# Performance work log

Measured on AMD Instinct MI355X. Metric: run time of the kernel, lower is better.

## Reference

```python
import jax, jax.numpy as jnp
import numpy as np

N, C, H, NG = 200000, 256, 4, 512
D = C // H  # head_dim = 64


def setup_inputs() -> dict:
    key = jax.random.key(0)
    ks = jax.random.split(key, 10)
    s = 1.0 / np.sqrt(C)
    inp = {
        "x": jax.random.normal(ks[0], (N, C), dtype=jnp.float32),
        "batch": jnp.sort(jax.random.randint(ks[1], (N,), 0, NG)),
        "Wq": jax.random.uniform(ks[2], (C, C), jnp.float32, -s, s),
        "bq": jnp.zeros((C,), jnp.float32),
        "Wk": jax.random.uniform(ks[3], (C, C), jnp.float32, -s, s),
        "bk": jnp.zeros((C,), jnp.float32),
        "Wv": jax.random.uniform(ks[4], (C, C), jnp.float32, -s, s),
        "bv": jnp.zeros((C,), jnp.float32),
        "Wo": jax.random.uniform(ks[5], (C, C), jnp.float32, -s, s),
        "bo": jnp.zeros((C,), jnp.float32),
    }
    return inp


def reference(x, batch, Wq, bq, Wk, bk, Wv, bv, Wo, bo):
    n = x.shape[0]
    q = (x @ Wq + bq).reshape(n, H, D)
    k = (x @ Wk + bk).reshape(n, H, D)
    v = (x @ Wv + bv).reshape(n, H, D)
    # per-node head-vs-head scores: [N, H, H]
    scores = jnp.einsum("nhd,ngd->nhg", q, k) / jnp.sqrt(jnp.float32(D))
    # segment softmax across nodes within each graph (torch_geometric.utils.softmax)
    seg_max = jax.ops.segment_max(scores, batch, num_segments=NG)
    e = jnp.exp(scores - seg_max[batch])
    seg_sum = jax.ops.segment_sum(e, batch, num_segments=NG)
    att = e / (seg_sum[batch] + 1e-16)
    out = jnp.einsum("nhg,ngd->nhd", att, v).reshape(n, C)
    out = out @ Wo + bo
    return (out, att.mean(axis=1))
```

## Files before the change

kernel.cpp:

```cpp
#include <hip/hip_runtime.h>

#define NN 200000
#define CC 256
#define NG 512

typedef __attribute__((ext_vector_type(8))) __bf16 bf16x8;
typedef __attribute__((ext_vector_type(16))) float f32x16;

typedef unsigned short u16;

#define VWAITN(n) asm volatile("s_waitcnt vmcnt(%0)" :: "i"(n) : "memory")
#define LWAIT0()  asm volatile("s_waitcnt lgkmcnt(0)" ::: "memory")
#define SBAR() __builtin_amdgcn_s_barrier()

__device__ __forceinline__ u16 f2bf(float f) {
  union { float f; unsigned u; } v; v.f = f;
  unsigned u = v.u;
  u += 0x7fffu + ((u >> 16) & 1u);
  return (u16)(u >> 16);
}
__device__ __forceinline__ unsigned pack2(float a, float b) {
  return (unsigned)f2bf(a) | ((unsigned)f2bf(b) << 16);
}
__device__ __forceinline__ float bflo(unsigned u){ union{unsigned u; float f;} x; x.u = u << 16; return x.f; }
__device__ __forceinline__ float bfhi(unsigned u){ union{unsigned u; float f;} x; x.u = u & 0xffff0000u; return x.f; }

__global__ __launch_bounds__(256) void prep_kernel(
    const float* __restrict__ Wq, const float* __restrict__ Wk,
    const float* __restrict__ Wv, const float* __restrict__ Wo,
    u16* __restrict__ Wall) {
  int idx = blockIdx.x * 256 + threadIdx.x;
  int s = idx >> 13;
  int inner = idx & 8191;
  int ks = inner >> 9;
  int l = (inner >> 3) & 63;
  int j = inner & 7;
  int r = l & 31, hi5 = l >> 5;
  int k = ks * 16 + hi5 * 8 + j;
  const float* W; int c0;
  if (s < 16) {
    int p = s >> 3, r4 = s & 7;
    if (r4 < 4) { W = Wk; c0 = r4 * 64 + p * 32; }
    else        { W = Wq; c0 = (r4 - 4) * 64 + p * 32; }
  } else if (s < 24) { W = Wv; c0 = (s - 16) * 32; }
  else               { W = Wo; c0 = (s - 24) * 32; }
  Wall[idx] = f2bf(W[k * 256 + c0 + r]);
}

__global__ __launch_bounds__(256) void seg_bounds_kernel(
    const int* __restrict__ batch, int* __restrict__ seg_start, int n) {
  int i = blockIdx.x * 256 + threadIdx.x;
  if (i >= n) return;
  int a = batch[i];
  int b = (i + 1 < n) ? batch[i + 1] : NG;
  for (int g = a + 1; g <= b; ++g) seg_start[g] = i + 1;
  if (i == 0) for (int g = 0; g <= a; ++g) seg_start[g] = 0;
}

__device__ __forceinline__ void stage_pair(
    const u16* __restrict__ Wall, u16* dst_base, int s0, int w, int lane) {
#pragma unroll
  for (int rep = 0; rep < 8; ++rep) {
    int unit = w * 8 + rep;
    const u16* src = Wall + (size_t)s0 * 8192 + (unit * 64 + lane) * 8;
    u16* dst = dst_base + unit * 512;
    __builtin_amdgcn_global_load_lds(
        (const __attribute__((address_space(1))) void*)src,
        (__attribute__((address_space(3))) void*)dst, 16, 0, 0);
  }
}

__device__ __forceinline__ f32x16 gemm_lds(
    const u16* buf, const bf16x8 xfr[16], int lane) {
  f32x16 a0 = {0.f,0.f,0.f,0.f,0.f,0.f,0.f,0.f,0.f,0.f,0.f,0.f,0.f,0.f,0.f,0.f};
  f32x16 a1 = a0;
#pragma unroll
  for (int ks = 0; ks < 16; ks += 2) {
    bf16x8 f0 = *reinterpret_cast<const bf16x8*>(&buf[(ks * 64 + lane) * 8]);
    bf16x8 f1 = *reinterpret_cast<const bf16x8*>(&buf[((ks + 1) * 64 + lane) * 8]);
    a0 = __builtin_amdgcn_mfma_f32_32x32x16_bf16(f0, xfr[ks], a0, 0, 0, 0);
    a1 = __builtin_amdgcn_mfma_f32_32x32x16_bf16(f1, xfr[ks + 1], a1, 0, 0, 0);
  }
  return a0 + a1;
}

__global__ __launch_bounds__(256, 2) void qkv_scores_kernel(
    const float* __restrict__ x, const u16* __restrict__ Wall,
    const float* __restrict__ bq, const float* __restrict__ bk,
    const float* __restrict__ bv,
    u16* __restrict__ v_out,
    float* __restrict__ scores) {
  __shared__ u16 Wbuf[2][16384];
  __shared__ float biasL[768];

  const int t = threadIdx.x;
  const int w = t >> 6, lane = t & 63;
  const int col = lane & 31, hi5 = lane >> 5;
  int n = blockIdx.x * 128 + w * 32 + col;
  if (n >= NN) n = NN - 1;

  bf16x8 xfr[16];
#pragma unroll
  for (int kb = 0; kb < 16; ++kb) {
    const float* px = x + (size_t)n * CC + kb * 16 + hi5 * 8;
    float4 a0 = *reinterpret_cast<const float4*>(px);
    float4 a1 = *reinterpret_cast<const float4*>(px + 4);
    uint4 u = {pack2(a0.x, a0.y), pack2(a0.z, a0.w),
               pack2(a1.x, a1.y), pack2(a1.z, a1.w)};
    xfr[kb] = *reinterpret_cast<bf16x8*>(&u);
  }
  biasL[t] = bk[t];
  biasL[256 + t] = bq[t];
  biasL[512 + t] = bv[t];

  stage_pair(Wall, Wbuf[0], 0, w, lane);
  LWAIT0();

  float sp[16];
#pragma unroll
  for (int i = 0; i < 16; ++i) sp[i] = 0.f;

  int bi = 0;

#pragma unroll 1
  for (int p = 0; p < 2; ++p) {
    unsigned kph[4][8];
#pragma unroll
    for (int pr = 0; pr < 2; ++pr) {
      VWAITN(0);
      SBAR();
      stage_pair(Wall, Wbuf[bi ^ 1], (p * 4 + pr + 1) * 2, w, lane);
#pragma unroll
      for (int sub = 0; sub < 2; ++sub) {
        const int g = pr * 2 + sub;
        f32x16 acc = gemm_lds(&Wbuf[bi][sub * 8192], xfr, lane);
#pragma unroll
        for (int q = 0; q < 4; ++q) {
          float4 b4 = *reinterpret_cast<const float4*>(
              &biasL[g * 64 + p * 32 + q * 8 + hi5 * 4]);
          kph[g][q * 2]     = pack2(acc[4 * q] + b4.x, acc[4 * q + 1] + b4.y);
          kph[g][q * 2 + 1] = pack2(acc[4 * q + 2] + b4.z, acc[4 * q + 3] + b4.w);
        }
      }
      bi ^= 1;
    }
#pragma unroll
    for (int pr = 0; pr < 2; ++pr) {
      VWAITN(0);
      SBAR();
      stage_pair(Wall, Wbuf[bi ^ 1], (p * 4 + 3 + pr) * 2, w, lane);
#pragma unroll
      for (int sub = 0; sub < 2; ++sub) {
        const int h = pr * 2 + sub;
        f32x16 acc = gemm_lds(&Wbuf[bi][sub * 8192], xfr, lane);
#pragma unroll
        for (int q = 0; q < 4; ++q) {
          float4 b4 = *reinterpret_cast<const float4*>(
              &biasL[256 + h * 64 + p * 32 + q * 8 + hi5 * 4]);
          float q0 = acc[4 * q] + b4.x, q1 = acc[4 * q + 1] + b4.y;
          float q2 = acc[4 * q + 2] + b4.z, q3 = acc[4 * q + 3] + b4.w;
#pragma unroll
          for (int g = 0; g < 4; ++g) {
            unsigned k01 = kph[g][q * 2];
            unsigned k23 = kph[g][q * 2 + 1];
            sp[h * 4 + g] += q0 * bflo(k01) + q1 * bfhi(k01) +
                             q2 * bflo(k23) + q3 * bfhi(k23);
          }
        }
      }
      bi ^= 1;
    }
  }

#pragma unroll
  for (int i = 0; i < 16; ++i) sp[i] += __shfl_xor(sp[i], 32, 64);
  if (hi5 == 0) {
#pragma unroll
    for (int q = 0; q < 4; ++q) {
      float4 o = {sp[q * 4] * 0.125f, sp[q * 4 + 1] * 0.125f,
                  sp[q * 4 + 2] * 0.125f, sp[q * 4 + 3] * 0.125f};
      *reinterpret_cast<float4*>(scores + (size_t)n * 16 + q * 4) = o;
    }
  }

#pragma unroll
  for (int i = 0; i < 4; ++i) {
    if (i == 0) { VWAITN(4); }
    else        { VWAITN(8); }
    SBAR();
    if (i < 3) stage_pair(Wall, Wbuf[bi ^ 1], 18 + 2 * i, w, lane);
#pragma unroll
    for (int sub = 0; sub < 2; ++sub) {
      const int sv = 2 * i + sub;
      f32x16 acc = gemm_lds(&Wbuf[bi][sub * 8192], xfr, lane);
#pragma unroll
      for (int q = 0; q < 4; ++q) {
        int d0 = sv * 32 + q * 8 + hi5 * 4;
        float4 b4 = *reinterpret_cast<const float4*>(&biasL[512 + d0]);
        uint2 pk = {pack2(acc[4 * q] + b4.x, acc[4 * q + 1] + b4.y),
                    pack2(acc[4 * q + 2] + b4.z, acc[4 * q + 3] + b4.w)};
        *reinterpret_cast<uint2*>(v_out + (size_t)n * CC + d0) = pk;
      }
    }
    bi ^= 1;
  }
}

__global__ __launch_bounds__(256) void seg_softmax_kernel(
    const float* __restrict__ scores, const int* __restrict__ seg_start,
    float* __restrict__ seg_max, float* __restrict__ seg_sum) {
  __shared__ float red[256];
  int g = blockIdx.x;
  int s = seg_start[g], e = seg_start[g + 1];
  int t = threadIdx.x;
  int col = t & 15, sub = t >> 4;

  float m = -INFINITY;
  for (int i = s + sub; i < e; i += 16)
    m = fmaxf(m, scores[(size_t)i * 16 + col]);
  red[t] = m;
  __syncthreads();
  for (int step = 8; step >= 1; step >>= 1) {
    if (sub < step) red[t] = fmaxf(red[t], red[t + step * 16]);
    __syncthreads();
  }
  if (t < 16) seg_max[g * 16 + t] = red[t];
  float mcol = red[col];
  __syncthreads();

  float sum = 0.f;
  for (int i = s + sub; i < e; i += 16)
    sum += expf(scores[(size_t)i * 16 + col] - mcol);
  red[t] = sum;
  __syncthreads();
  for (int step = 8; step >= 1; step >>= 1) {
    if (sub < step) red[t] += red[t + step * 16];
    __syncthreads();
  }
  if (t < 16) seg_sum[g * 16 + t] = red[t];
}

__global__ __launch_bounds__(256, 2) void out_kernel(
    const u16* __restrict__ v_bf, const float* __restrict__ scores,
    const int* __restrict__ batch, const float* __restrict__ seg_max,
    const float* __restrict__ seg_sum, const u16* __restrict__ Wall,
    const float* __restrict__ bo, float* __restrict__ out,
    float* __restrict__ att_mean) {
  __shared__ u16 Wbuf[2][16384];
  __shared__ float boL[256];

  const int t = threadIdx.x;
  const int w = t >> 6, lane = t & 63;
  const int col = lane & 31, hi5 = lane >> 5;
  int n = blockIdx.x * 128 + w * 32 + col;
  if (n >= NN) n = NN - 1;

  int b = batch[n];
  float att[16];
#pragma unroll
  for (int q = 0; q < 4; ++q) {
    float4 sc = *reinterpret_cast<const float4*>(scores + (size_t)n * 16 + q * 4);
    float4 mx = *reinterpret_cast<const float4*>(seg_max + b * 16 + q * 4);
    float4 sm = *reinterpret_cast<const float4*>(seg_sum + b * 16 + q * 4);
    att[q * 4 + 0] = expf(sc.x - mx.x) / (sm.x + 1e-16f);
    att[q * 4 + 1] = expf(sc.y - mx.y) / (sm.y + 1e-16f);
    att[q * 4 + 2] = expf(sc.z - mx.z) / (sm.z + 1e-16f);
    att[q * 4 + 3] = expf(sc.w - mx.w) / (sm.w + 1e-16f);
  }

  uint4 vv[4][4];
#pragma unroll
  for (int g = 0; g < 4; ++g)
#pragma unroll
    for (int dw = 0; dw < 4; ++dw)
      vv[g][dw] = *reinterpret_cast<const uint4*>(
          v_bf + (size_t)n * CC + g * 64 + dw * 16 + hi5 * 8);

  boL[t] = bo[t];

  if (hi5 == 0) {
    float4 am;
    am.x = 0.25f * (att[0] + att[4] + att[8] + att[12]);
    am.y = 0.25f * (att[1] + att[5] + att[9] + att[13]);
    am.z = 0.25f * (att[2] + att[6] + att[10] + att[14]);
    am.w = 0.25f * (att[3] + att[7] + att[11] + att[15]);
    *reinterpret_cast<float4*>(att_mean + (size_t)n * 4) = am;
  }

  stage_pair(Wall, Wbuf[0], 24, w, lane);

  bf16x8 oaf[16];
#pragma unroll
  for (int dw = 0; dw < 4; ++dw) {
    float vr[4][8];
#pragma unroll
    for (int g = 0; g < 4; ++g) {
      uint4 u4 = vv[g][dw];
      vr[g][0] = bflo(u4.x); vr[g][1] = bfhi(u4.x);
      vr[g][2] = bflo(u4.y); vr[g][3] = bfhi(u4.y);
      vr[g][4] = bflo(u4.z); vr[g][5] = bfhi(u4.z);
      vr[g][6] = bflo(u4.w); vr[g][7] = bfhi(u4.w);
    }
#pragma unroll
    for (int h = 0; h < 4; ++h) {
      unsigned res[4];
#pragma unroll
      for (int jj = 0; jj < 4; ++jj) {
        float lo = att[h * 4 + 0] * vr[0][2 * jj] + att[h * 4 + 1] * vr[1][2 * jj] +
                   att[h * 4 + 2] * vr[2][2 * jj] + att[h * 4 + 3] * vr[3][2 * jj];
        float hf = att[h * 4 + 0] * vr[0][2 * jj + 1] + att[h * 4 + 1] * vr[1][2 * jj + 1] +
                   att[h * 4 + 2] * vr[2][2 * jj + 1] + att[h * 4 + 3] * vr[3][2 * jj + 1];
        res[jj] = pack2(lo, hf);
      }
      uint4 u = {res[0], res[1], res[2], res[3]};
      oaf[h * 4 + dw] = *reinterpret_cast<bf16x8*>(&u);
    }
  }
  LWAIT0();

  int bi = 0;
#pragma unroll
  for (int i = 0; i < 4; ++i) {
    if (i == 0) { VWAITN(0); }
    else        { VWAITN(8); }
    SBAR();
    if (i < 3) stage_pair(Wall, Wbuf[bi ^ 1], 26 + 2 * i, w, lane);
#pragma unroll
    for (int sub = 0; sub < 2; ++sub) {
      const int so = 2 * i + sub;
      f32x16 acc = gemm_lds(&Wbuf[bi][sub * 8192], oaf, lane);
#pragma unroll
      for (int q = 0; q < 4; ++q) {
        int c0 = so * 32 + q * 8 + hi5 * 4;
        float4 b4 = *reinterpret_cast<const float4*>(&boL[c0]);
        float4 o = {acc[4 * q] + b4.x, acc[4 * q + 1] + b4.y,
                    acc[4 * q + 2] + b4.z, acc[4 * q + 3] + b4.w};
        *reinterpret_cast<float4*>(out + (size_t)n * CC + c0) = o;
      }
    }
    bi ^= 1;
  }
}

extern "C" void kernel_launch(void* const* d_in, const int* in_sizes, int n_in,
                              void* d_out, int out_size, void* d_ws, size_t ws_size,
                              hipStream_t stream) {
  const float* x  = (const float*)d_in[0];
  const int* batch = (const int*)d_in[1];
  const float* Wq = (const float*)d_in[2];
  const float* bq = (const float*)d_in[3];
  const float* Wk = (const float*)d_in[4];
  const float* bk = (const float*)d_in[5];
  const float* Wv = (const float*)d_in[6];
  const float* bv = (const float*)d_in[7];
  const float* Wo = (const float*)d_in[8];
  const float* bo = (const float*)d_in[9];

  char* ws = (char*)d_ws;
  u16*   Wall      = (u16*)ws;
  int*   seg_start = (int*)(ws + 524288);
  float* seg_max   = (float*)(ws + 528384);
  float* seg_sum   = (float*)(ws + 561152);
  float* scores    = (float*)(ws + 593920);
  u16*   v_bf      = (u16*)(ws + 13393920);

  float* out = (float*)d_out;
  float* att_mean = out + (size_t)NN * CC;

  const int NB = (NN + 127) / 128;

  prep_kernel<<<1024, 256, 0, stream>>>(Wq, Wk, Wv, Wo, Wall);
  seg_bounds_kernel<<<(NN + 255) / 256, 256, 0, stream>>>(batch, seg_start, NN);
  qkv_scores_kernel<<<NB, 256, 0, stream>>>(x, Wall, bq, bk, bv, v_bf, scores);
  seg_softmax_kernel<<<NG, 256, 0, stream>>>(scores, seg_start, seg_max, seg_sum);
  out_kernel<<<NB, 256, 0, stream>>>(v_bf, scores, batch, seg_max, seg_sum,
                                     Wall, bo, out, att_mean);
}
```

Measured before the change: 259.1 us.

## Switch QKV and output GEMMs to 16x16x32 MFMA with 512-thread blocks

Both the QKV/score kernel and the output-projection kernel now use 16x16x32 bf16 MFMA tiles instead of 32x32x16, with 8 waves of 16 nodes per 128-node block instead of 4 waves of 32. The weight pre-packing is relaid out to match the new fragment layout, and the LDS staging is spread across all 512 threads. Per-thread register state shrinks, since the x fragment count, the K-partials and the V registers are halved, and a second shuffle step completes the score reduction. The aim is more resident waves and better latency hiding for a bandwidth-heavy kernel. The cost is more MFMA instructions and more LDS fragment reads per output, plus tighter vmcnt bookkeeping.

```diff
diff --git a/kernel.cpp b/kernel.cpp
--- a/kernel.cpp
+++ b/kernel.cpp
@@ -5,7 +5,7 @@
 #define NG 512
 
 typedef __attribute__((ext_vector_type(8))) __bf16 bf16x8;
-typedef __attribute__((ext_vector_type(16))) float f32x16;
+typedef __attribute__((ext_vector_type(4))) float f32x4;
 
 typedef unsigned short u16;
 
@@ -31,12 +31,13 @@
     u16* __restrict__ Wall) {
   int idx = blockIdx.x * 256 + threadIdx.x;
   int s = idx >> 13;
-  int inner = idx & 8191;
-  int ks = inner >> 9;
-  int l = (inner >> 3) & 63;
-  int j = inner & 7;
-  int r = l & 31, hi5 = l >> 5;
-  int k = ks * 16 + hi5 * 8 + j;
+  int r1 = idx & 8191;
+  int sub = r1 >> 12;
+  int r2 = r1 & 4095;
+  int ks = r2 >> 9;
+  int lane = (r2 >> 3) & 63;
+  int j = r2 & 7;
+  int k = ks * 32 + (lane >> 4) * 8 + j;
   const float* W; int c0;
   if (s < 16) {
     int p = s >> 3, r4 = s & 7;
@@ -44,7 +45,7 @@
     else        { W = Wq; c0 = (r4 - 4) * 64 + p * 32; }
   } else if (s < 24) { W = Wv; c0 = (s - 16) * 32; }
   else               { W = Wo; c0 = (s - 24) * 32; }
-  Wall[idx] = f2bf(W[k * 256 + c0 + r]);
+  Wall[idx] = f2bf(W[k * 256 + c0 + sub * 16 + (lane & 15)]);
 }
 
 __global__ __launch_bounds__(256) void seg_bounds_kernel(
@@ -58,33 +59,30 @@
 }
 
 __device__ __forceinline__ void stage_pair(
-    const u16* __restrict__ Wall, u16* dst_base, int s0, int w, int lane) {
-#pragma unroll
-  for (int rep = 0; rep < 8; ++rep) {
-    int unit = w * 8 + rep;
-    const u16* src = Wall + (size_t)s0 * 8192 + (unit * 64 + lane) * 8;
-    u16* dst = dst_base + unit * 512;
+    const u16* __restrict__ Wall, u16* dst_base, int s0, int t) {
+#pragma unroll
+  for (int rep = 0; rep < 4; ++rep) {
+    int unit = rep * 512 + t;
+    const u16* src = Wall + (size_t)s0 * 8192 + unit * 8;
+    u16* dst = dst_base + unit * 8;
     __builtin_amdgcn_global_load_lds(
         (const __attribute__((address_space(1))) void*)src,
         (__attribute__((address_space(3))) void*)dst, 16, 0, 0);
   }
 }
 
-__device__ __forceinline__ f32x16 gemm_lds(
-    const u16* buf, const bf16x8 xfr[16], int lane) {
-  f32x16 a0 = {0.f,0.f,0.f,0.f,0.f,0.f,0.f,0.f,0.f,0.f,0.f,0.f,0.f,0.f,0.f,0.f};
-  f32x16 a1 = a0;
-#pragma unroll
-  for (int ks = 0; ks < 16; ks += 2) {
-    bf16x8 f0 = *reinterpret_cast<const bf16x8*>(&buf[(ks * 64 + lane) * 8]);
-    bf16x8 f1 = *reinterpret_cast<const bf16x8*>(&buf[((ks + 1) * 64 + lane) * 8]);
-    a0 = __builtin_amdgcn_mfma_f32_32x32x16_bf16(f0, xfr[ks], a0, 0, 0, 0);
-    a1 = __builtin_amdgcn_mfma_f32_32x32x16_bf16(f1, xfr[ks + 1], a1, 0, 0, 0);
-  }
-  return a0 + a1;
-}
-
-__global__ __launch_bounds__(256, 2) void qkv_scores_kernel(
+__device__ __forceinline__ f32x4 gemm16(
+    const u16* buf, const bf16x8 xfr[8], int lane) {
+  f32x4 acc = {0.f, 0.f, 0.f, 0.f};
+#pragma unroll
+  for (int ks = 0; ks < 8; ++ks) {
+    bf16x8 af = *reinterpret_cast<const bf16x8*>(&buf[ks * 512 + lane * 8]);
+    acc = __builtin_amdgcn_mfma_f32_16x16x32_bf16(af, xfr[ks], acc, 0, 0, 0);
+  }
+  return acc;
+}
+
+__global__ __launch_bounds__(512, 4) void qkv_scores_kernel(
     const float* __restrict__ x, const u16* __restrict__ Wall,
     const float* __restrict__ bq, const float* __restrict__ bk,
     const float* __restrict__ bv,
@@ -95,25 +93,25 @@
 
   const int t = threadIdx.x;
   const int w = t >> 6, lane = t & 63;
-  const int col = lane & 31, hi5 = lane >> 5;
-  int n = blockIdx.x * 128 + w * 32 + col;
+  const int g4 = lane >> 4;
+  int n = blockIdx.x * 128 + w * 16 + (lane & 15);
   if (n >= NN) n = NN - 1;
 
-  bf16x8 xfr[16];
-#pragma unroll
-  for (int kb = 0; kb < 16; ++kb) {
-    const float* px = x + (size_t)n * CC + kb * 16 + hi5 * 8;
+  bf16x8 xfr[8];
+#pragma unroll
+  for (int ks = 0; ks < 8; ++ks) {
+    const float* px = x + (size_t)n * CC + ks * 32 + g4 * 8;
     float4 a0 = *reinterpret_cast<const float4*>(px);
     float4 a1 = *reinterpret_cast<const float4*>(px + 4);
     uint4 u = {pack2(a0.x, a0.y), pack2(a0.z, a0.w),
                pack2(a1.x, a1.y), pack2(a1.z, a1.w)};
-    xfr[kb] = *reinterpret_cast<bf16x8*>(&u);
-  }
-  biasL[t] = bk[t];
-  biasL[256 + t] = bq[t];
-  biasL[512 + t] = bv[t];
-
-  stage_pair(Wall, Wbuf[0], 0, w, lane);
+    xfr[ks] = *reinterpret_cast<bf16x8*>(&u);
+  }
+  biasL[t < 256 ? t : t] = 0.f;
+  if (t < 256) { biasL[t] = bk[t]; biasL[512 + t] = bv[t]; }
+  else         { biasL[t] = bq[t - 256]; }
+
+  stage_pair(Wall, Wbuf[0], 0, t);
   LWAIT0();
 
   float sp[16];
@@ -124,47 +122,51 @@
 
 #pragma unroll 1
   for (int p = 0; p < 2; ++p) {
-    unsigned kph[4][8];
+    unsigned kph[4][4];
 #pragma unroll
     for (int pr = 0; pr < 2; ++pr) {
+      const int s0 = p * 8 + pr * 2;
       VWAITN(0);
       SBAR();
-      stage_pair(Wall, Wbuf[bi ^ 1], (p * 4 + pr + 1) * 2, w, lane);
-#pragma unroll
-      for (int sub = 0; sub < 2; ++sub) {
-        const int g = pr * 2 + sub;
-        f32x16 acc = gemm_lds(&Wbuf[bi][sub * 8192], xfr, lane);
-#pragma unroll
-        for (int q = 0; q < 4; ++q) {
+      stage_pair(Wall, Wbuf[bi ^ 1], s0 + 2, t);
+#pragma unroll
+      for (int so = 0; so < 2; ++so) {
+        const int g = pr * 2 + so;
+#pragma unroll
+        for (int sub = 0; sub < 2; ++sub) {
+          f32x4 acc = gemm16(&Wbuf[bi][so * 8192 + sub * 4096], xfr, lane);
           float4 b4 = *reinterpret_cast<const float4*>(
-              &biasL[g * 64 + p * 32 + q * 8 + hi5 * 4]);
-          kph[g][q * 2]     = pack2(acc[4 * q] + b4.x, acc[4 * q + 1] + b4.y);
-          kph[g][q * 2 + 1] = pack2(acc[4 * q + 2] + b4.z, acc[4 * q + 3] + b4.w);
+              &biasL[g * 64 + p * 32 + sub * 16 + g4 * 4]);
+          kph[g][sub * 2]     = pack2(acc[0] + b4.x, acc[1] + b4.y);
+          kph[g][sub * 2 + 1] = pack2(acc[2] + b4.z, acc[3] + b4.w);
         }
       }
       bi ^= 1;
     }
 #pragma unroll
     for (int pr = 0; pr < 2; ++pr) {
+      const int s0 = p * 8 + 4 + pr * 2;
       VWAITN(0);
       SBAR();
-      stage_pair(Wall, Wbuf[bi ^ 1], (p * 4 + 3 + pr) * 2, w, lane);
-#pragma unroll
-      for (int sub = 0; sub < 2; ++sub) {
-        const int h = pr * 2 + sub;
-        f32x16 acc = gemm_lds(&Wbuf[bi][sub * 8192], xfr, lane);
-#pragma unroll
-        for (int q = 0; q < 4; ++q) {
+      stage_pair(Wall, Wbuf[bi ^ 1], s0 + 2, t);
+#pragma unroll
+      for (int so = 0; so < 2; ++so) {
+        const int h = pr * 2 + so;
+#pragma unroll
+        for (int sub = 0; sub < 2; ++sub) {
+          f32x4 acc = gemm16(&Wbuf[bi][so * 8192 + sub * 4096], xfr, lane);
           float4 b4 = *reinterpret_cast<const float4*>(
-              &biasL[256 + h * 64 + p * 32 + q * 8 + hi5 * 4]);
-          float q0 = acc[4 * q] + b4.x, q1 = acc[4 * q + 1] + b4.y;
-          float q2 = acc[4 * q + 2] + b4.z, q3 = acc[4 * q + 3] + b4.w;
-#pragma unroll
-          for (int g = 0; g < 4; ++g) {
-            unsigned k01 = kph[g][q * 2];
-            unsigned k23 = kph[g][q * 2 + 1];
-            sp[h * 4 + g] += q0 * bflo(k01) + q1 * bfhi(k01) +
-                             q2 * bflo(k23) + q3 * bfhi(k23);
+              &biasL[256 + h * 64 + p * 32 + sub * 16 + g4 * 4]);
+          float qv[4] = {acc[0] + b4.x, acc[1] + b4.y,
+                         acc[2] + b4.z, acc[3] + b4.w};
+#pragma unroll
+          for (int r = 0; r < 4; ++r) {
+#pragma unroll
+            for (int g = 0; g < 4; ++g) {
+              unsigned kk = kph[g][sub * 2 + (r >> 1)];
+              float kv = (r & 1) ? bfhi(kk) : bflo(kk);
+              sp[h * 4 + g] += qv[r] * kv;
+            }
           }
         }
       }
@@ -173,8 +175,11 @@
   }
 
 #pragma unroll
-  for (int i = 0; i < 16; ++i) sp[i] += __shfl_xor(sp[i], 32, 64);
-  if (hi5 == 0) {
+  for (int i = 0; i < 16; ++i) {
+    sp[i] += __shfl_xor(sp[i], 16, 64);
+    sp[i] += __shfl_xor(sp[i], 32, 64);
+  }
+  if (lane < 16) {
 #pragma unroll
     for (int q = 0; q < 4; ++q) {
       float4 o = {sp[q * 4] * 0.125f, sp[q * 4 + 1] * 0.125f,
@@ -185,20 +190,20 @@
 
 #pragma unroll
   for (int i = 0; i < 4; ++i) {
-    if (i == 0) { VWAITN(4); }
-    else        { VWAITN(8); }
+    const int s0 = 16 + 2 * i;
+    VWAITN(4);
     SBAR();
-    if (i < 3) stage_pair(Wall, Wbuf[bi ^ 1], 18 + 2 * i, w, lane);
-#pragma unroll
-    for (int sub = 0; sub < 2; ++sub) {
-      const int sv = 2 * i + sub;
-      f32x16 acc = gemm_lds(&Wbuf[bi][sub * 8192], xfr, lane);
-#pragma unroll
-      for (int q = 0; q < 4; ++q) {
-        int d0 = sv * 32 + q * 8 + hi5 * 4;
+    if (i < 3) stage_pair(Wall, Wbuf[bi ^ 1], s0 + 2, t);
+#pragma unroll
+    for (int so = 0; so < 2; ++so) {
+      const int sv = 2 * i + so;
+#pragma unroll
+      for (int sub = 0; sub < 2; ++sub) {
+        f32x4 acc = gemm16(&Wbuf[bi][so * 8192 + sub * 4096], xfr, lane);
+        int d0 = sv * 32 + sub * 16 + g4 * 4;
         float4 b4 = *reinterpret_cast<const float4*>(&biasL[512 + d0]);
-        uint2 pk = {pack2(acc[4 * q] + b4.x, acc[4 * q + 1] + b4.y),
-                    pack2(acc[4 * q + 2] + b4.z, acc[4 * q + 3] + b4.w)};
+        uint2 pk = {pack2(acc[0] + b4.x, acc[1] + b4.y),
+                    pack2(acc[2] + b4.z, acc[3] + b4.w)};
         *reinterpret_cast<uint2*>(v_out + (size_t)n * CC + d0) = pk;
       }
     }
@@ -240,7 +245,7 @@
   if (t < 16) seg_sum[g * 16 + t] = red[t];
 }
 
-__global__ __launch_bounds__(256, 2) void out_kernel(
+__global__ __launch_bounds__(512, 4) void out_kernel(
     const u16* __restrict__ v_bf, const float* __restrict__ scores,
     const int* __restrict__ batch, const float* __restrict__ seg_max,
     const float* __restrict__ seg_sum, const u16* __restrict__ Wall,
@@ -251,8 +256,8 @@
 
   const int t = threadIdx.x;
   const int w = t >> 6, lane = t & 63;
-  const int col = lane & 31, hi5 = lane >> 5;
-  int n = blockIdx.x * 128 + w * 32 + col;
+  const int g4 = lane >> 4;
+  int n = blockIdx.x * 128 + w * 16 + (lane & 15);
   if (n >= NN) n = NN - 1;
 
   int b = batch[n];
@@ -268,17 +273,9 @@
     att[q * 4 + 3] = expf(sc.w - mx.w) / (sm.w + 1e-16f);
   }
 
-  uint4 vv[4][4];
-#pragma unroll
-  for (int g = 0; g < 4; ++g)
-#pragma unroll
-    for (int dw = 0; dw < 4; ++dw)
-      vv[g][dw] = *reinterpret_cast<const uint4*>(
-          v_bf + (size_t)n * CC + g * 64 + dw * 16 + hi5 * 8);
-
-  boL[t] = bo[t];
-
-  if (hi5 == 0) {
+  if (t < 256) boL[t] = bo[t];
+
+  if (lane < 16) {
     float4 am;
     am.x = 0.25f * (att[0] + att[4] + att[8] + att[12]);
     am.y = 0.25f * (att[1] + att[5] + att[9] + att[13]);
@@ -287,34 +284,35 @@
     *reinterpret_cast<float4*>(att_mean + (size_t)n * 4) = am;
   }
 
-  stage_pair(Wall, Wbuf[0], 24, w, lane);
-
-  bf16x8 oaf[16];
-#pragma unroll
-  for (int dw = 0; dw < 4; ++dw) {
-    float vr[4][8];
-#pragma unroll
-    for (int g = 0; g < 4; ++g) {
-      uint4 u4 = vv[g][dw];
-      vr[g][0] = bflo(u4.x); vr[g][1] = bfhi(u4.x);
-      vr[g][2] = bflo(u4.y); vr[g][3] = bfhi(u4.y);
-      vr[g][4] = bflo(u4.z); vr[g][5] = bfhi(u4.z);
-      vr[g][6] = bflo(u4.w); vr[g][7] = bfhi(u4.w);
-    }
-#pragma unroll
-    for (int h = 0; h < 4; ++h) {
-      unsigned res[4];
-#pragma unroll
-      for (int jj = 0; jj < 4; ++jj) {
-        float lo = att[h * 4 + 0] * vr[0][2 * jj] + att[h * 4 + 1] * vr[1][2 * jj] +
-                   att[h * 4 + 2] * vr[2][2 * jj] + att[h * 4 + 3] * vr[3][2 * jj];
-        float hf = att[h * 4 + 0] * vr[0][2 * jj + 1] + att[h * 4 + 1] * vr[1][2 * jj + 1] +
-                   att[h * 4 + 2] * vr[2][2 * jj + 1] + att[h * 4 + 3] * vr[3][2 * jj + 1];
-        res[jj] = pack2(lo, hf);
-      }
-      uint4 u = {res[0], res[1], res[2], res[3]};
-      oaf[h * 4 + dw] = *reinterpret_cast<bf16x8*>(&u);
-    }
+  uint4 vv[4][2];
+#pragma unroll
+  for (int g = 0; g < 4; ++g)
+#pragma unroll
+    for (int par = 0; par < 2; ++par)
+      vv[g][par] = *reinterpret_cast<const uint4*>(
+          v_bf + (size_t)n * CC + g * 64 + par * 32 + g4 * 8);
+
+  stage_pair(Wall, Wbuf[0], 24, t);
+
+  bf16x8 oaf[8];
+#pragma unroll
+  for (int ks = 0; ks < 8; ++ks) {
+    const int h = ks >> 1, par = ks & 1;
+    unsigned res[4];
+#pragma unroll
+    for (int jj = 0; jj < 4; ++jj) {
+      unsigned u0 = ((const unsigned*)&vv[0][par])[jj];
+      unsigned u1 = ((const unsigned*)&vv[1][par])[jj];
+      unsigned u2 = ((const unsigned*)&vv[2][par])[jj];
+      unsigned u3 = ((const unsigned*)&vv[3][par])[jj];
+      float lo = att[h * 4 + 0] * bflo(u0) + att[h * 4 + 1] * bflo(u1) +
+                 att[h * 4 + 2] * bflo(u2) + att[h * 4 + 3] * bflo(u3);
+      float hf = att[h * 4 + 0] * bfhi(u0) + att[h * 4 + 1] * bfhi(u1) +
+                 att[h * 4 + 2] * bfhi(u2) + att[h * 4 + 3] * bfhi(u3);
+      res[jj] = pack2(lo, hf);
+    }
+    uint4 u = {res[0], res[1], res[2], res[3]};
+    oaf[ks] = *reinterpret_cast<bf16x8*>(&u);
   }
   LWAIT0();
 
@@ -322,19 +320,19 @@
 #pragma unroll
   for (int i = 0; i < 4; ++i) {
     if (i == 0) { VWAITN(0); }
-    else        { VWAITN(8); }
+    else        { VWAITN(4); }
     SBAR();
-    if (i < 3) stage_pair(Wall, Wbuf[bi ^ 1], 26 + 2 * i, w, lane);
-#pragma unroll
-    for (int sub = 0; sub < 2; ++sub) {
-      const int so = 2 * i + sub;
-      f32x16 acc = gemm_lds(&Wbuf[bi][sub * 8192], oaf, lane);
-#pragma unroll
-      for (int q = 0; q < 4; ++q) {
-        int c0 = so * 32 + q * 8 + hi5 * 4;
+    if (i < 3) stage_pair(Wall, Wbuf[bi ^ 1], 26 + 2 * i, t);
+#pragma unroll
+    for (int so = 0; so < 2; ++so) {
+      const int sl = 2 * i + so;
+#pragma unroll
+      for (int sub = 0; sub < 2; ++sub) {
+        f32x4 acc = gemm16(&Wbuf[bi][so * 8192 + sub * 4096], oaf, lane);
+        int c0 = sl * 32 + sub * 16 + g4 * 4;
         float4 b4 = *reinterpret_cast<const float4*>(&boL[c0]);
-        float4 o = {acc[4 * q] + b4.x, acc[4 * q + 1] + b4.y,
-                    acc[4 * q + 2] + b4.z, acc[4 * q + 3] + b4.w};
+        float4 o = {acc[0] + b4.x, acc[1] + b4.y,
+                    acc[2] + b4.z, acc[3] + b4.w};
         *reinterpret_cast<float4*>(out + (size_t)n * CC + c0) = o;
       }
     }
@@ -371,8 +369,8 @@
 
   prep_kernel<<<1024, 256, 0, stream>>>(Wq, Wk, Wv, Wo, Wall);
   seg_bounds_kernel<<<(NN + 255) / 256, 256, 0, stream>>>(batch, seg_start, NN);
-  qkv_scores_kernel<<<NB, 256, 0, stream>>>(x, Wall, bq, bk, bv, v_bf, scores);
+  qkv_scores_kernel<<<NB, 512, 0, stream>>>(x, Wall, bq, bk, bv, v_bf, scores);
   seg_softmax_kernel<<<NG, 256, 0, stream>>>(scores, seg_start, seg_max, seg_sum);
-  out_kernel<<<NB, 256, 0, stream>>>(v_bf, scores, batch, seg_max, seg_sum,
+  out_kernel<<<NB, 512, 0, stream>>>(v_bf, scores, batch, seg_max, seg_sum,
                                      Wall, bo, out, att_mean);
 }
```

New measurement: 277.1 us. +6.9%, slower.

## Split V projection into separate 16x16 MFMA kernel and merge seg-bounds into prep

Applied to the files above, without the earlier changes.

Moves the V projection out of the fused QK-scores kernel into its own kernel, which uses 512-thread blocks, 16x16x32 MFMAs and a Wv layout repacked for that shape. The QK kernel then holds fewer live registers and skips the now-unneeded final Wv stage. The segment-bounds computation is folded into the weight-prep launch to save one kernel launch. In exchange, x is read from global memory twice (once per kernel), adding roughly 200 MB of extra traffic.

```diff
diff --git a/kernel.cpp b/kernel.cpp
--- a/kernel.cpp
+++ b/kernel.cpp
@@ -6,6 +6,7 @@
 
 typedef __attribute__((ext_vector_type(8))) __bf16 bf16x8;
 typedef __attribute__((ext_vector_type(16))) float f32x16;
+typedef __attribute__((ext_vector_type(4))) float f32x4;
 
 typedef unsigned short u16;
 
@@ -28,36 +29,48 @@
 __global__ __launch_bounds__(256) void prep_kernel(
     const float* __restrict__ Wq, const float* __restrict__ Wk,
     const float* __restrict__ Wv, const float* __restrict__ Wo,
-    u16* __restrict__ Wall) {
-  int idx = blockIdx.x * 256 + threadIdx.x;
+    u16* __restrict__ Wall,
+    const int* __restrict__ batch, int* __restrict__ seg_start) {
+  int bidx = blockIdx.x;
+  if (bidx >= 1024) {
+    int i = (bidx - 1024) * 256 + threadIdx.x;
+    if (i >= NN) return;
+    int a = batch[i];
+    int b = (i + 1 < NN) ? batch[i + 1] : NG;
+    for (int g = a + 1; g <= b; ++g) seg_start[g] = i + 1;
+    if (i == 0) for (int g = 0; g <= a; ++g) seg_start[g] = 0;
+    return;
+  }
+  int idx = bidx * 256 + threadIdx.x;
   int s = idx >> 13;
-  int inner = idx & 8191;
-  int ks = inner >> 9;
-  int l = (inner >> 3) & 63;
-  int j = inner & 7;
-  int r = l & 31, hi5 = l >> 5;
-  int k = ks * 16 + hi5 * 8 + j;
-  const float* W; int c0;
-  if (s < 16) {
-    int p = s >> 3, r4 = s & 7;
-    if (r4 < 4) { W = Wk; c0 = r4 * 64 + p * 32; }
-    else        { W = Wq; c0 = (r4 - 4) * 64 + p * 32; }
-  } else if (s < 24) { W = Wv; c0 = (s - 16) * 32; }
-  else               { W = Wo; c0 = (s - 24) * 32; }
-  Wall[idx] = f2bf(W[k * 256 + c0 + r]);
-}
-
-__global__ __launch_bounds__(256) void seg_bounds_kernel(
-    const int* __restrict__ batch, int* __restrict__ seg_start, int n) {
-  int i = blockIdx.x * 256 + threadIdx.x;
-  if (i >= n) return;
-  int a = batch[i];
-  int b = (i + 1 < n) ? batch[i + 1] : NG;
-  for (int g = a + 1; g <= b; ++g) seg_start[g] = i + 1;
-  if (i == 0) for (int g = 0; g <= a; ++g) seg_start[g] = 0;
-}
-
-__device__ __forceinline__ void stage_pair(
+  if (s >= 16 && s < 24) {
+    int r1 = idx & 8191;
+    int sub = r1 >> 12;
+    int r2 = r1 & 4095;
+    int ks = r2 >> 9;
+    int lane = (r2 >> 3) & 63;
+    int j = r2 & 7;
+    int k = ks * 32 + (lane >> 4) * 8 + j;
+    int c0 = (s - 16) * 32;
+    Wall[idx] = f2bf(Wv[k * 256 + c0 + sub * 16 + (lane & 15)]);
+  } else {
+    int inner = idx & 8191;
+    int ks = inner >> 9;
+    int l = (inner >> 3) & 63;
+    int j = inner & 7;
+    int r = l & 31, hi5 = l >> 5;
+    int k = ks * 16 + hi5 * 8 + j;
+    const float* W; int c0;
+    if (s < 16) {
+      int p = s >> 3, r4 = s & 7;
+      if (r4 < 4) { W = Wk; c0 = r4 * 64 + p * 32; }
+      else        { W = Wq; c0 = (r4 - 4) * 64 + p * 32; }
+    } else { W = Wo; c0 = (s - 24) * 32; }
+    Wall[idx] = f2bf(W[k * 256 + c0 + r]);
+  }
+}
+
+__device__ __forceinline__ void stage_pair4(
     const u16* __restrict__ Wall, u16* dst_base, int s0, int w, int lane) {
 #pragma unroll
   for (int rep = 0; rep < 8; ++rep) {
@@ -70,6 +83,19 @@
   }
 }
 
+__device__ __forceinline__ void stage_pair8(
+    const u16* __restrict__ Wall, u16* dst_base, int s0, int t) {
+#pragma unroll
+  for (int rep = 0; rep < 4; ++rep) {
+    int unit = rep * 512 + t;
+    const u16* src = Wall + (size_t)s0 * 8192 + unit * 8;
+    u16* dst = dst_base + unit * 8;
+    __builtin_amdgcn_global_load_lds(
+        (const __attribute__((address_space(1))) void*)src,
+        (__attribute__((address_space(3))) void*)dst, 16, 0, 0);
+  }
+}
+
 __device__ __forceinline__ f32x16 gemm_lds(
     const u16* buf, const bf16x8 xfr[16], int lane) {
   f32x16 a0 = {0.f,0.f,0.f,0.f,0.f,0.f,0.f,0.f,0.f,0.f,0.f,0.f,0.f,0.f,0.f,0.f};
@@ -84,19 +110,28 @@
   return a0 + a1;
 }
 
-__global__ __launch_bounds__(256, 2) void qkv_scores_kernel(
+__device__ __forceinline__ f32x4 gemm16(
+    const u16* buf, const bf16x8 xfr[8], int lane) {
+  f32x4 acc = {0.f, 0.f, 0.f, 0.f};
+#pragma unroll
+  for (int ks = 0; ks < 8; ++ks) {
+    bf16x8 af = *reinterpret_cast<const bf16x8*>(&buf[ks * 512 + lane * 8]);
+    acc = __builtin_amdgcn_mfma_f32_16x16x32_bf16(af, xfr[ks], acc, 0, 0, 0);
+  }
+  return acc;
+}
+
+__global__ __launch_bounds__(256, 2) void qk_scores_kernel(
     const float* __restrict__ x, const u16* __restrict__ Wall,
     const float* __restrict__ bq, const float* __restrict__ bk,
-    const float* __restrict__ bv,
-    u16* __restrict__ v_out,
     float* __restrict__ scores) {
   __shared__ u16 Wbuf[2][16384];
-  __shared__ float biasL[768];
+  __shared__ float biasL[512];
 
   const int t = threadIdx.x;
   const int w = t >> 6, lane = t & 63;
-  const int col = lane & 31, hi5 = lane >> 5;
-  int n = blockIdx.x * 128 + w * 32 + col;
+  const int hi5 = lane >> 5;
+  int n = blockIdx.x * 128 + w * 32 + (lane & 31);
   if (n >= NN) n = NN - 1;
 
   bf16x8 xfr[16];
@@ -111,9 +146,8 @@
   }
   biasL[t] = bk[t];
   biasL[256 + t] = bq[t];
-  biasL[512 + t] = bv[t];
-
-  stage_pair(Wall, Wbuf[0], 0, w, lane);
+
+  stage_pair4(Wall, Wbuf[0], 0, w, lane);
   LWAIT0();
 
   float sp[16];
@@ -129,7 +163,7 @@
     for (int pr = 0; pr < 2; ++pr) {
       VWAITN(0);
       SBAR();
-      stage_pair(Wall, Wbuf[bi ^ 1], (p * 4 + pr + 1) * 2, w, lane);
+      stage_pair4(Wall, Wbuf[bi ^ 1], (p * 4 + pr + 1) * 2, w, lane);
 #pragma unroll
       for (int sub = 0; sub < 2; ++sub) {
         const int g = pr * 2 + sub;
@@ -148,7 +182,8 @@
     for (int pr = 0; pr < 2; ++pr) {
       VWAITN(0);
       SBAR();
-      stage_pair(Wall, Wbuf[bi ^ 1], (p * 4 + 3 + pr) * 2, w, lane);
+      if (p == 0 || pr == 0)
+        stage_pair4(Wall, Wbuf[bi ^ 1], (p * 4 + 3 + pr) * 2, w, lane);
 #pragma unroll
       for (int sub = 0; sub < 2; ++sub) {
         const int h = pr * 2 + sub;
@@ -182,23 +217,53 @@
       *reinterpret_cast<float4*>(scores + (size_t)n * 16 + q * 4) = o;
     }
   }
-
+}
+
+__global__ __launch_bounds__(512, 4) void v_proj_kernel(
+    const float* __restrict__ x, const u16* __restrict__ Wall,
+    const float* __restrict__ bv,
+    u16* __restrict__ v_out) {
+  __shared__ u16 Wbuf[2][16384];
+  __shared__ float bvL[256];
+
+  const int t = threadIdx.x;
+  const int w = t >> 6, lane = t & 63;
+  const int g4 = lane >> 4;
+  int n = blockIdx.x * 128 + w * 16 + (lane & 15);
+  if (n >= NN) n = NN - 1;
+
+  bf16x8 xfr[8];
+#pragma unroll
+  for (int ks = 0; ks < 8; ++ks) {
+    const float* px = x + (size_t)n * CC + ks * 32 + g4 * 8;
+    float4 a0 = *reinterpret_cast<const float4*>(px);
+    float4 a1 = *reinterpret_cast<const float4*>(px + 4);
+    uint4 u = {pack2(a0.x, a0.y), pack2(a0.z, a0.w),
+               pack2(a1.x, a1.y), pack2(a1.z, a1.w)};
+    xfr[ks] = *reinterpret_cast<bf16x8*>(&u);
+  }
+  if (t < 256) bvL[t] = bv[t];
+
+  stage_pair8(Wall, Wbuf[0], 16, t);
+  LWAIT0();
+
+  int bi = 0;
 #pragma unroll
   for (int i = 0; i < 4; ++i) {
-    if (i == 0) { VWAITN(4); }
-    else        { VWAITN(8); }
+    if (i == 0) { VWAITN(0); }
+    else        { VWAITN(4); }
     SBAR();
-    if (i < 3) stage_pair(Wall, Wbuf[bi ^ 1], 18 + 2 * i, w, lane);
-#pragma unroll
-    for (int sub = 0; sub < 2; ++sub) {
-      const int sv = 2 * i + sub;
-      f32x16 acc = gemm_lds(&Wbuf[bi][sub * 8192], xfr, lane);
-#pragma unroll
-      for (int q = 0; q < 4; ++q) {
-        int d0 = sv * 32 + q * 8 + hi5 * 4;
-        float4 b4 = *reinterpret_cast<const float4*>(&biasL[512 + d0]);
-        uint2 pk = {pack2(acc[4 * q] + b4.x, acc[4 * q + 1] + b4.y),
-                    pack2(acc[4 * q + 2] + b4.z, acc[4 * q + 3] + b4.w)};
+    if (i < 3) stage_pair8(Wall, Wbuf[bi ^ 1], 18 + 2 * i, t);
+#pragma unroll
+    for (int so = 0; so < 2; ++so) {
+      const int sv = 2 * i + so;
+#pragma unroll
+      for (int sub = 0; sub < 2; ++sub) {
+        f32x4 acc = gemm16(&Wbuf[bi][so * 8192 + sub * 4096], xfr, lane);
+        int d0 = sv * 32 + sub * 16 + g4 * 4;
+        float4 b4 = *reinterpret_cast<const float4*>(&bvL[d0]);
+        uint2 pk = {pack2(acc[0] + b4.x, acc[1] + b4.y),
+                    pack2(acc[2] + b4.z, acc[3] + b4.w)};
         *reinterpret_cast<uint2*>(v_out + (size_t)n * CC + d0) = pk;
       }
     }
@@ -251,8 +316,8 @@
 
   const int t = threadIdx.x;
   const int w = t >> 6, lane = t & 63;
-  const int col = lane & 31, hi5 = lane >> 5;
-  int n = blockIdx.x * 128 + w * 32 + col;
+  const int hi5 = lane >> 5;
+  int n = blockIdx.x * 128 + w * 32 + (lane & 31);
   if (n >= NN) n = NN - 1;
 
   int b = batch[n];
@@ -287,7 +352,7 @@
     *reinterpret_cast<float4*>(att_mean + (size_t)n * 4) = am;
   }
 
-  stage_pair(Wall, Wbuf[0], 24, w, lane);
+  stage_pair4(Wall, Wbuf[0], 24, w, lane);
 
   bf16x8 oaf[16];
 #pragma unroll
@@ -324,14 +389,14 @@
     if (i == 0) { VWAITN(0); }
     else        { VWAITN(8); }
     SBAR();
-    if (i < 3) stage_pair(Wall, Wbuf[bi ^ 1], 26 + 2 * i, w, lane);
-#pragma unroll
-    for (int sub = 0; sub < 2; ++sub) {
-      const int so = 2 * i + sub;
-      f32x16 acc = gemm_lds(&Wbuf[bi][sub * 8192], oaf, lane);
+    if (i < 3) stage_pair4(Wall, Wbuf[bi ^ 1], 26 + 2 * i, w, lane);
+#pragma unroll
+    for (int so = 0; so < 2; ++so) {
+      const int sl = 2 * i + so;
+      f32x16 acc = gemm_lds(&Wbuf[bi][so * 8192], oaf, lane);
 #pragma unroll
       for (int q = 0; q < 4; ++q) {
-        int c0 = so * 32 + q * 8 + hi5 * 4;
+        int c0 = sl * 32 + q * 8 + hi5 * 4;
         float4 b4 = *reinterpret_cast<const float4*>(&boL[c0]);
         float4 o = {acc[4 * q] + b4.x, acc[4 * q + 1] + b4.y,
                     acc[4 * q + 2] + b4.z, acc[4 * q + 3] + b4.w};
@@ -369,9 +434,10 @@
 
   const int NB = (NN + 127) / 128;
 
-  prep_kernel<<<1024, 256, 0, stream>>>(Wq, Wk, Wv, Wo, Wall);
-  seg_bounds_kernel<<<(NN + 255) / 256, 256, 0, stream>>>(batch, seg_start, NN);
-  qkv_scores_kernel<<<NB, 256, 0, stream>>>(x, Wall, bq, bk, bv, v_bf, scores);
+  prep_kernel<<<1024 + (NN + 255) / 256, 256, 0, stream>>>(
+      Wq, Wk, Wv, Wo, Wall, batch, seg_start);
+  qk_scores_kernel<<<NB, 256, 0, stream>>>(x, Wall, bq, bk, scores);
+  v_proj_kernel<<<NB, 512, 0, stream>>>(x, Wall, bv, v_bf);
   seg_softmax_kernel<<<NG, 256, 0, stream>>>(scores, seg_start, seg_max, seg_sum);
   out_kernel<<<NB, 256, 0, stream>>>(v_bf, scores, batch, seg_max, seg_sum,
                                      Wall, bo, out, att_mean);
```

Result: slower. 476.5 us (+83.9%).
